# Kernel tuning notes

Measured on AMD Instinct MI355X. Metric: run time of the kernel, lower is better.

Reference implementation:

```python
import jax, jax.numpy as jnp
import numpy as np

N_NODES = 50000


def setup_inputs() -> dict:
    key = jax.random.key(0)
    k1, k2, k3, k4 = jax.random.split(key, 4)
    N, E, F_IN, F_OUT = N_NODES, 1600000, 512, 128
    x = jax.random.normal(k1, (N, F_IN), dtype=jnp.float32)
    edge_index = jax.random.randint(k2, (2, E), 0, N, dtype=jnp.int64)
    edge_weight = jax.random.uniform(k3, (E,), dtype=jnp.float32)
    # glorot init for weight, zeros bias (as in the original layer)
    limit = np.sqrt(6.0 / (F_IN + F_OUT)).astype(np.float32)
    weight = jax.random.uniform(k4, (F_IN, F_OUT), dtype=jnp.float32,
                                minval=-limit, maxval=limit)
    bias = jnp.zeros((F_OUT,), dtype=jnp.float32)
    return {"x": x, "edge_index": edge_index, "edge_weight": edge_weight,
            "weight": weight, "bias": bias}


def reference(x, edge_index, edge_weight, weight, bias):
    # dropout rate is 0 in this config -> identity
    h = x @ weight                                # [N, F_out] dense transform
    src, dst = edge_index[0], edge_index[1]
    # support @ h : sparse adjacency aggregation (SpMM) via gather + segment_sum
    msgs = h[src] * edge_weight[:, None]          # [E, F_out]
    agg = jax.ops.segment_sum(msgs, dst, num_segments=N_NODES)  # [N, F_out]
    return jax.nn.relu(agg + bias)
```

## Files before the change

kernel.cpp:

```cpp
#include <hip/hip_runtime.h>

#define F_IN  512
#define F_OUT 128
#define FBIN  32
#define EPB   8192
#define C2MAX 1600
#define CAPF  2048

typedef __attribute__((ext_vector_type(8))) short  short8;
typedef __attribute__((ext_vector_type(4))) float  floatx4;

__device__ __forceinline__ unsigned short f2bf(float f) {
    unsigned u = __float_as_uint(f);
    return (unsigned short)((u + 0x7FFF + ((u >> 16) & 1)) >> 16);
}
__device__ __forceinline__ float bf2f(unsigned b) {
    return __uint_as_float(b << 16);
}

__global__ __launch_bounds__(256) void prep(
    const float* __restrict__ w, unsigned short* __restrict__ wt,
    int* __restrict__ cursor, int C2)
{
    const int tid = threadIdx.x;
    if ((int)blockIdx.x < 128) {
        int g0 = blockIdx.x * 512 + tid;
        #pragma unroll
        for (int r = 0; r < 2; ++r) {
            int gid = g0 + r * 256;
            int n = gid >> 9, k = gid & 511;
            wt[gid] = f2bf(w[(size_t)k * F_OUT + n]);
        }
    } else {
        int c = ((int)blockIdx.x - 128) * 256 + tid;
        if (c < C2) cursor[c] = 0;
    }
}

__global__ __launch_bounds__(512, 1) void fill_gemm(
    const int* __restrict__ ei, const float* __restrict__ ew,
    int* __restrict__ cursor, uint2* __restrict__ ent, int E, int C2, int FB,
    const float* __restrict__ x, const unsigned short* __restrict__ wt,
    unsigned short* __restrict__ h, int N)
{
    __shared__ __align__(16) char smem[(128 * 68 + 128 * 68) * 2];
    const int tid = threadIdx.x;

    if ((int)blockIdx.x < FB) {
        int* lh    = (int*)smem;
        int* lbase = (int*)smem + C2MAX;
        for (int c = tid; c < C2; c += 512) lh[c] = 0;
        __syncthreads();

        const int base = blockIdx.x * EPB;
        unsigned       mykey[EPB / 512];
        unsigned char  mydl[EPB / 512];
        short          mybin[EPB / 512];
        unsigned short myrank[EPB / 512];

        #pragma unroll
        for (int j = 0; j < EPB / 512; ++j) {
            int e = base + j * 512 + tid;
            mybin[j] = -1;
            if (e < E) {
                int   src = ei[e];
                int   dst = ei[E + e];
                float w   = ew[e];
                int bin = dst >> 5;
                mykey[j]  = (unsigned)src | ((unsigned)f2bf(w) << 16);
                mydl[j]   = (unsigned char)(dst & (FBIN - 1));
                mybin[j]  = (short)bin;
                myrank[j] = (unsigned short)atomicAdd(&lh[bin], 1);
            }
        }
        __syncthreads();
        for (int c = tid; c < C2; c += 512)
            if (lh[c] > 0) lbase[c] = atomicAdd(&cursor[c], lh[c]);
        __syncthreads();
        #pragma unroll
        for (int j = 0; j < EPB / 512; ++j) {
            if (mybin[j] >= 0) {
                int o = lbase[mybin[j]] + myrank[j];
                if (o < CAPF)
                    ent[(size_t)(int)mybin[j] * CAPF + o] = make_uint2(mykey[j], mydl[j]);
            }
        }
        return;
    }

    unsigned short* sa = (unsigned short*)smem;
    unsigned short* sb = sa + 128 * 68;

    const int wave = tid >> 6, lane = tid & 63;
    const int wm   = wave >> 1, wn = wave & 1;
    const int g    = lane >> 4, l16 = lane & 15;
    const int m0   = ((int)blockIdx.x - FB) * 128;

    const int arow = tid >> 2, aq = tid & 3;
    const int brow = tid >> 2, bq = tid & 3;

    floatx4 acc[2][4];
    #pragma unroll
    for (int rt = 0; rt < 2; ++rt)
        #pragma unroll
        for (int nt = 0; nt < 4; ++nt) acc[rt][nt] = (floatx4)(0.f);

    const bool  avalid = (m0 + arow) < N;
    const float* xp = x + (size_t)(m0 + arow) * F_IN + aq * 16;
    const unsigned short* bp = wt + brow * F_IN + bq * 16;

    float4 ax[4];
    uint4  bv[2];
    #pragma unroll
    for (int i = 0; i < 4; ++i) ax[i] = make_float4(0.f, 0.f, 0.f, 0.f);
    if (avalid) {
        #pragma unroll
        for (int i = 0; i < 4; ++i) ax[i] = ((const float4*)xp)[i];
    }
    #pragma unroll
    for (int i = 0; i < 2; ++i) bv[i] = ((const uint4*)bp)[i];

    for (int s = 0; s < 8; ++s) {
        __syncthreads();
        #pragma unroll
        for (int i = 0; i < 4; ++i) {
            ushort4 t;
            t.x = f2bf(ax[i].x); t.y = f2bf(ax[i].y);
            t.z = f2bf(ax[i].z); t.w = f2bf(ax[i].w);
            *(ushort4*)&sa[arow * 68 + aq * 16 + i * 4] = t;
        }
        #pragma unroll
        for (int i = 0; i < 2; ++i) {
            *(uint2*)&sb[brow * 68 + bq * 16 + i * 8]     = make_uint2(bv[i].x, bv[i].y);
            *(uint2*)&sb[brow * 68 + bq * 16 + i * 8 + 4] = make_uint2(bv[i].z, bv[i].w);
        }
        if (s < 7) {
            int k0n = (s + 1) * 64;
            if (avalid) {
                #pragma unroll
                for (int i = 0; i < 4; ++i) ax[i] = ((const float4*)(xp + k0n))[i];
            }
            #pragma unroll
            for (int i = 0; i < 2; ++i) bv[i] = ((const uint4*)(bp + k0n))[i];
        }
        __syncthreads();

        #pragma unroll
        for (int kc = 0; kc < 2; ++kc) {
            union { ushort4 u[2]; short8 v; } af[2];
            #pragma unroll
            for (int rt = 0; rt < 2; ++rt) {
                int abase = (wm * 32 + rt * 16 + l16) * 68 + kc * 32 + g * 8;
                af[rt].u[0] = *(ushort4*)&sa[abase];
                af[rt].u[1] = *(ushort4*)&sa[abase + 4];
            }
            #pragma unroll
            for (int nt = 0; nt < 4; ++nt) {
                union { ushort4 u[2]; short8 v; } bf;
                int bbase = (wn * 64 + nt * 16 + l16) * 68 + kc * 32 + g * 8;
                bf.u[0] = *(ushort4*)&sb[bbase];
                bf.u[1] = *(ushort4*)&sb[bbase + 4];
                #pragma unroll
                for (int rt = 0; rt < 2; ++rt)
                    acc[rt][nt] = __builtin_amdgcn_mfma_f32_16x16x32_bf16(
                        af[rt].v, bf.v, acc[rt][nt], 0, 0, 0);
            }
        }
    }

    #pragma unroll
    for (int rt = 0; rt < 2; ++rt) {
        #pragma unroll
        for (int nt = 0; nt < 4; ++nt) {
            #pragma unroll
            for (int r = 0; r < 4; ++r) {
                int row = m0 + wm * 32 + rt * 16 + g * 4 + r;
                int col = wn * 64 + nt * 16 + l16;
                if (row < N) h[(size_t)row * F_OUT + col] = f2bf(acc[rt][nt][r]);
            }
        }
    }
}

__global__ __launch_bounds__(256) void fine_agg(
    const unsigned short* __restrict__ h, const uint2* __restrict__ ent,
    const int* __restrict__ cursor, const float* __restrict__ bias,
    float* __restrict__ out, int N, int E,
    const int* __restrict__ ei, const float* __restrict__ ew)
{
    __shared__ unsigned ssort[CAPF];
    __shared__ int lh[FBIN], lcur[FBIN];
    __shared__ int sso[FBIN + 1];

    const int b    = blockIdx.x;
    const int tid  = threadIdx.x;
    const int wave = tid >> 6;
    const int lane = tid & 63;
    const int slot = lane >> 4;
    const int q    = lane & 15;
    const float4 bv0 = *(const float4*)&bias[q * 8];
    const float4 bv1 = *(const float4*)&bias[q * 8 + 4];
    const int raw  = cursor[b];
    const int cnt  = raw < CAPF ? raw : CAPF;
    const uint2* slab = ent + (size_t)b * CAPF;

    if (tid < FBIN) lh[tid] = 0;
    __syncthreads();

    for (int i = tid; i < cnt; i += 256)
        atomicAdd(&lh[(int)slab[i].y], 1);
    __syncthreads();

    if (wave == 0 && lane < FBIN) {
        int v = lh[lane];
        int orig = v;
        #pragma unroll
        for (int off = 1; off < FBIN; off <<= 1) {
            int t = __shfl_up(v, off);
            if (lane >= off) v += t;
        }
        sso[lane]  = v - orig;
        lcur[lane] = v - orig;
        if (lane == FBIN - 1) sso[FBIN] = v;
    }
    __syncthreads();

    if (raw <= CAPF) {
        for (int i = tid; i < cnt; i += 256) {
            uint2 e = slab[i];
            int r = atomicAdd(&lcur[(int)e.y], 1);
            ssort[r] = e.x;
        }
        __syncthreads();

        #pragma unroll 1
        for (int t = 0; t < 8; ++t) {
            int nd   = wave * 8 + t;
            int node = b * FBIN + nd;
            int s = sso[nd], e2 = sso[nd + 1];
            float4 a0 = make_float4(0.f, 0.f, 0.f, 0.f);
            float4 a1 = make_float4(0.f, 0.f, 0.f, 0.f);
            for (int i = s; i < e2; i += 16) {
                #pragma unroll
                for (int j = 0; j < 4; ++j) {
                    int idx = i + j * 4 + slot;
                    unsigned bk = 0;
                    if (idx < e2) bk = ssort[idx];
                    float wgt = bf2f(bk >> 16);
                    uint4 hv = *(const uint4*)&h[(size_t)(bk & 0xFFFF) * F_OUT + q * 8];
                    a0.x += bf2f(hv.x & 0xFFFF) * wgt;
                    a0.y += bf2f(hv.x >> 16)    * wgt;
                    a0.z += bf2f(hv.y & 0xFFFF) * wgt;
                    a0.w += bf2f(hv.y >> 16)    * wgt;
                    a1.x += bf2f(hv.z & 0xFFFF) * wgt;
                    a1.y += bf2f(hv.z >> 16)    * wgt;
                    a1.z += bf2f(hv.w & 0xFFFF) * wgt;
                    a1.w += bf2f(hv.w >> 16)    * wgt;
                }
            }
            a0.x += __shfl_xor(a0.x, 16);
            a0.y += __shfl_xor(a0.y, 16);
            a0.z += __shfl_xor(a0.z, 16);
            a0.w += __shfl_xor(a0.w, 16);
            a1.x += __shfl_xor(a1.x, 16);
            a1.y += __shfl_xor(a1.y, 16);
            a1.z += __shfl_xor(a1.z, 16);
            a1.w += __shfl_xor(a1.w, 16);
            a0.x += __shfl_xor(a0.x, 32);
            a0.y += __shfl_xor(a0.y, 32);
            a0.z += __shfl_xor(a0.z, 32);
            a0.w += __shfl_xor(a0.w, 32);
            a1.x += __shfl_xor(a1.x, 32);
            a1.y += __shfl_xor(a1.y, 32);
            a1.z += __shfl_xor(a1.z, 32);
            a1.w += __shfl_xor(a1.w, 32);
            if (slot == 0 && node < N) {
                float4 o0, o1;
                o0.x = fmaxf(a0.x + bv0.x, 0.f);
                o0.y = fmaxf(a0.y + bv0.y, 0.f);
                o0.z = fmaxf(a0.z + bv0.z, 0.f);
                o0.w = fmaxf(a0.w + bv0.w, 0.f);
                o1.x = fmaxf(a1.x + bv1.x, 0.f);
                o1.y = fmaxf(a1.y + bv1.y, 0.f);
                o1.z = fmaxf(a1.z + bv1.z, 0.f);
                o1.w = fmaxf(a1.w + bv1.w, 0.f);
                *(float4*)&out[(size_t)node * F_OUT + q * 8]     = o0;
                *(float4*)&out[(size_t)node * F_OUT + q * 8 + 4] = o1;
            }
        }
    } else {
        #pragma unroll 1
        for (int t = 0; t < 8; ++t) {
            int nd   = wave * 8 + t;
            int node = b * FBIN + nd;
            float4 a0 = make_float4(0.f, 0.f, 0.f, 0.f);
            float4 a1 = make_float4(0.f, 0.f, 0.f, 0.f);
            for (int e = slot; e < E; e += 4) {
                if (ei[E + e] == node) {
                    float wgt = ew[e];
                    uint4 hv = *(const uint4*)&h[(size_t)ei[e] * F_OUT + q * 8];
                    a0.x += bf2f(hv.x & 0xFFFF) * wgt;
                    a0.y += bf2f(hv.x >> 16)    * wgt;
                    a0.z += bf2f(hv.y & 0xFFFF) * wgt;
                    a0.w += bf2f(hv.y >> 16)    * wgt;
                    a1.x += bf2f(hv.z & 0xFFFF) * wgt;
                    a1.y += bf2f(hv.z >> 16)    * wgt;
                    a1.z += bf2f(hv.w & 0xFFFF) * wgt;
                    a1.w += bf2f(hv.w >> 16)    * wgt;
                }
            }
            a0.x += __shfl_xor(a0.x, 16);
            a0.y += __shfl_xor(a0.y, 16);
            a0.z += __shfl_xor(a0.z, 16);
            a0.w += __shfl_xor(a0.w, 16);
            a1.x += __shfl_xor(a1.x, 16);
            a1.y += __shfl_xor(a1.y, 16);
            a1.z += __shfl_xor(a1.z, 16);
            a1.w += __shfl_xor(a1.w, 16);
            a0.x += __shfl_xor(a0.x, 32);
            a0.y += __shfl_xor(a0.y, 32);
            a0.z += __shfl_xor(a0.z, 32);
            a0.w += __shfl_xor(a0.w, 32);
            a1.x += __shfl_xor(a1.x, 32);
            a1.y += __shfl_xor(a1.y, 32);
            a1.z += __shfl_xor(a1.z, 32);
            a1.w += __shfl_xor(a1.w, 32);
            if (slot == 0 && node < N) {
                float4 o0, o1;
                o0.x = fmaxf(a0.x + bv0.x, 0.f);
                o0.y = fmaxf(a0.y + bv0.y, 0.f);
                o0.z = fmaxf(a0.z + bv0.z, 0.f);
                o0.w = fmaxf(a0.w + bv0.w, 0.f);
                o1.x = fmaxf(a1.x + bv1.x, 0.f);
                o1.y = fmaxf(a1.y + bv1.y, 0.f);
                o1.z = fmaxf(a1.z + bv1.z, 0.f);
                o1.w = fmaxf(a1.w + bv1.w, 0.f);
                *(float4*)&out[(size_t)node * F_OUT + q * 8]     = o0;
                *(float4*)&out[(size_t)node * F_OUT + q * 8 + 4] = o1;
            }
        }
    }
}

static inline size_t align256(size_t x) { return (x + 255) & ~(size_t)255; }

extern "C" void kernel_launch(void* const* d_in, const int* in_sizes, int n_in,
                              void* d_out, int out_size, void* d_ws, size_t ws_size,
                              hipStream_t stream)
{
    const float* x    = (const float*)d_in[0];
    const int*   ei   = (const int*)  d_in[1];
    const float* ew   = (const float*)d_in[2];
    const float* w    = (const float*)d_in[3];
    const float* bias = (const float*)d_in[4];
    float*       out  = (float*)d_out;

    const int N  = in_sizes[0] / F_IN;
    const int E  = in_sizes[2];
    const int C2 = (N + FBIN - 1) / FBIN;

    char*  ws = (char*)d_ws;
    size_t off = 0;
    unsigned short* h      = (unsigned short*)(ws + off); off += align256((size_t)N * F_OUT * 2);
    unsigned short* wt     = (unsigned short*)(ws + off); off += align256((size_t)F_OUT * F_IN * 2);
    int*            cursor = (int*)(ws + off);            off += align256((size_t)C2 * 4);
    uint2*          ent    = (uint2*)(ws + off);          off += align256((size_t)C2 * CAPF * 8);

    const int FB = (E + EPB - 1) / EPB;
    const int GB = (N + 127) / 128;
    const int ZB = (C2 + 255) / 256;

    prep<<<128 + ZB, 256, 0, stream>>>(w, wt, cursor, C2);
    fill_gemm<<<FB + GB, 512, 0, stream>>>(ei, ew, cursor, ent, E, C2, FB,
                                           x, wt, h, N);
    fine_agg<<<C2, 256, 0, stream>>>(h, ent, cursor, bias, out, N, E, ei, ew);
}
```

Measured before the change: 252.5 us.

## Replace block-local bin counting with direct padded global atomics per edge

```diff
diff --git a/kernel.cpp b/kernel.cpp
--- a/kernel.cpp
+++ b/kernel.cpp
@@ -6,6 +6,7 @@
 #define EPB   8192
 #define C2MAX 1600
 #define CAPF  2048
+#define CPAD  16
 
 typedef __attribute__((ext_vector_type(8))) short  short8;
 typedef __attribute__((ext_vector_type(4))) float  floatx4;
@@ -33,7 +34,7 @@
         }
     } else {
         int c = ((int)blockIdx.x - 128) * 256 + tid;
-        if (c < C2) cursor[c] = 0;
+        if (c < C2 * CPAD) cursor[c] = 0;
     }
 }
 
@@ -47,42 +48,20 @@
     const int tid = threadIdx.x;
 
     if ((int)blockIdx.x < FB) {
-        int* lh    = (int*)smem;
-        int* lbase = (int*)smem + C2MAX;
-        for (int c = tid; c < C2; c += 512) lh[c] = 0;
-        __syncthreads();
-
         const int base = blockIdx.x * EPB;
-        unsigned       mykey[EPB / 512];
-        unsigned char  mydl[EPB / 512];
-        short          mybin[EPB / 512];
-        unsigned short myrank[EPB / 512];
-
-        #pragma unroll
+        #pragma unroll 4
         for (int j = 0; j < EPB / 512; ++j) {
             int e = base + j * 512 + tid;
-            mybin[j] = -1;
             if (e < E) {
                 int   src = ei[e];
                 int   dst = ei[E + e];
-                float w   = ew[e];
+                float wv  = ew[e];
                 int bin = dst >> 5;
-                mykey[j]  = (unsigned)src | ((unsigned)f2bf(w) << 16);
-                mydl[j]   = (unsigned char)(dst & (FBIN - 1));
-                mybin[j]  = (short)bin;
-                myrank[j] = (unsigned short)atomicAdd(&lh[bin], 1);
-            }
-        }
-        __syncthreads();
-        for (int c = tid; c < C2; c += 512)
-            if (lh[c] > 0) lbase[c] = atomicAdd(&cursor[c], lh[c]);
-        __syncthreads();
-        #pragma unroll
-        for (int j = 0; j < EPB / 512; ++j) {
-            if (mybin[j] >= 0) {
-                int o = lbase[mybin[j]] + myrank[j];
+                int o = atomicAdd(&cursor[bin * CPAD], 1);
                 if (o < CAPF)
-                    ent[(size_t)(int)mybin[j] * CAPF + o] = make_uint2(mykey[j], mydl[j]);
+                    ent[(size_t)bin * CAPF + o] = make_uint2(
+                        (unsigned)src | ((unsigned)f2bf(wv) << 16),
+                        (unsigned)(dst & (FBIN - 1)));
             }
         }
         return;
@@ -200,7 +179,7 @@
     const int q    = lane & 15;
     const float4 bv0 = *(const float4*)&bias[q * 8];
     const float4 bv1 = *(const float4*)&bias[q * 8 + 4];
-    const int raw  = cursor[b];
+    const int raw  = cursor[b * CPAD];
     const int cnt  = raw < CAPF ? raw : CAPF;
     const uint2* slab = ent + (size_t)b * CAPF;
 
@@ -363,12 +342,12 @@
     size_t off = 0;
     unsigned short* h      = (unsigned short*)(ws + off); off += align256((size_t)N * F_OUT * 2);
     unsigned short* wt     = (unsigned short*)(ws + off); off += align256((size_t)F_OUT * F_IN * 2);
-    int*            cursor = (int*)(ws + off);            off += align256((size_t)C2 * 4);
+    int*            cursor = (int*)(ws + off);            off += align256((size_t)C2 * CPAD * 4);
     uint2*          ent    = (uint2*)(ws + off);          off += align256((size_t)C2 * CAPF * 8);
 
     const int FB = (E + EPB - 1) / EPB;
     const int GB = (N + 127) / 128;
-    const int ZB = (C2 + 255) / 256;
+    const int ZB = (C2 * CPAD + 255) / 256;
 
     prep<<<128 + ZB, 256, 0, stream>>>(w, wt, cursor, C2);
     fill_gemm<<<FB + GB, 512, 0, stream>>>(ei, ew, cursor, ent, E, C2, FB,
```

New measurement: 284.3 us. 12.6% more time.
